# Kernel optimization log

Hardware: AMD Instinct MI355X
Metric: run time of the kernel (lower is better)

Reference implementation:

```python
import jax, jax.numpy as jnp
import numpy as np

N = 100000   # num nodes
E = 1600000  # num edges
D = 256      # input feature dim (dataset.num_features)


def setup_inputs() -> dict:
    key = jax.random.key(0)
    ks = jax.random.split(key, 10)

    def w(k, fan_in, fan_out):
        return jax.random.normal(k, (fan_in, fan_out), jnp.float32) / jnp.sqrt(fan_in)

    return {
        "x": jax.random.normal(ks[0], (N, D), jnp.float32),
        "edge_index": jax.random.randint(ks[1], (2, E), 0, N, jnp.int32),
        "W1": w(ks[2], D, 128),   "b1": jnp.zeros((128,), jnp.float32),
        "W2": w(ks[3], 128, 128), "b2": jnp.zeros((128,), jnp.float32),
        "W3": w(ks[4], 128, 64),  "b3": jnp.zeros((64,), jnp.float32),
        "W4": w(ks[5], 64, 32),   "b4": jnp.zeros((32,), jnp.float32),
    }


def _gcn_norm(edge_index, n):
    # GCNConv default: add self-loops, symmetric deg^-1/2 normalization
    loops = jnp.arange(n, dtype=edge_index.dtype)
    src = jnp.concatenate([edge_index[0], loops])
    dst = jnp.concatenate([edge_index[1], loops])
    deg = jax.ops.segment_sum(jnp.ones_like(dst, jnp.float32), dst, num_segments=n)
    dinv = jnp.where(deg > 0, jax.lax.rsqrt(deg), 0.0)
    norm = dinv[src] * dinv[dst]  # [E+N]
    return src, dst, norm


def _gcn_layer(x, W, b, src, dst, norm, n):
    h = x @ W                          # [N, out]
    msg = h[src] * norm[:, None]       # gather + scale: [E+N, out]
    agg = jax.ops.segment_sum(msg, dst, num_segments=n)  # scatter-add
    return agg + b


def reference(x, edge_index, W1, b1, W2, b2, W3, b3, W4, b4):
    n = x.shape[0]
    src, dst, norm = _gcn_norm(edge_index, n)
    h = jax.nn.relu(_gcn_layer(x, W1, b1, src, dst, norm, n))
    h = jax.nn.relu(_gcn_layer(h, W2, b2, src, dst, norm, n))
    h = jax.nn.relu(_gcn_layer(h, W3, b3, src, dst, norm, n))
    return _gcn_layer(h, W4, b4, src, dst, norm, n)  # encode() output z: [N, 32]
```

## Files before the change

### kernel.cpp

```cpp
#include <hip/hip_runtime.h>

#define CDIV(a,b) (((a)+(b)-1)/(b))
#define BUK_SHIFT 10
#define EPB 4096

typedef float f32x4 __attribute__((ext_vector_type(4)));
typedef short short8 __attribute__((ext_vector_type(8)));
typedef _Float16 h16x8 __attribute__((ext_vector_type(8)));


__device__ inline unsigned short rne_bf16(float f) {
    unsigned int u = __builtin_bit_cast(unsigned int, f);
    u += 0x7FFFu + ((u >> 16) & 1u);
    return (unsigned short)(u >> 16);
}

struct BF16Pair { short hi, lo; };

__device__ inline BF16Pair split_bf16(float f) {
    unsigned short h = rne_bf16(f);
    float fh = __builtin_bit_cast(float, (unsigned int)h << 16);
    BF16Pair p;
    p.hi = (short)h;
    p.lo = (short)rne_bf16(f - fh);
    return p;
}


__global__ __launch_bounds__(256) void bkt_hist_kernel(const int* __restrict__ dst,
                                                       int* __restrict__ hcnt,
                                                       int E, int nbuk, int nblk) {
    __shared__ int lh[128];
    int t = threadIdx.x;
    for (int i = t; i < nbuk; i += 256) lh[i] = 0;
    __syncthreads();
    int base = blockIdx.x * EPB;
    int end = min(base + EPB, E);
    for (int e = base + t; e < end; e += 256)
        atomicAdd(&lh[dst[e] >> BUK_SHIFT], 1);
    __syncthreads();
    for (int i = t; i < nbuk; i += 256) hcnt[i * nblk + blockIdx.x] = lh[i];
}

__global__ __launch_bounds__(1024) void scan_flat_kernel(int* a, int n) {
    __shared__ int s[1024];
    int t = threadIdx.x;
    int per = (n + 1023) / 1024;
    int start = t * per, end = min(start + per, n);
    int sum = 0;
    for (int i = start; i < end; ++i) sum += a[i];
    s[t] = sum;
    __syncthreads();
    for (int off = 1; off < 1024; off <<= 1) {
        int x = (t >= off) ? s[t - off] : 0;
        __syncthreads();
        s[t] += x;
        __syncthreads();
    }
    int run = s[t] - sum;
    for (int i = start; i < end; ++i) { int v = a[i]; a[i] = run; run += v; }
}

__global__ __launch_bounds__(256) void bkt_scatter_kernel(const int* __restrict__ src,
                                                          const int* __restrict__ dst,
                                                          const int* __restrict__ obk,
                                                          unsigned long long* __restrict__ ebuf,
                                                          int E, int nbuk, int nblk) {
    __shared__ int cur[128];
    int t = threadIdx.x;
    for (int i = t; i < nbuk; i += 256) cur[i] = obk[i * nblk + blockIdx.x];
    __syncthreads();
    int base = blockIdx.x * EPB;
    int end = min(base + EPB, E);
    for (int e = base + t; e < end; e += 256) {
        int d = dst[e], s = src[e];
        int b = d >> BUK_SHIFT;
        int pos = atomicAdd(&cur[b], 1);
        ebuf[pos] = ((unsigned long long)(unsigned)d << 32) | (unsigned)s;
    }
}

__global__ __launch_bounds__(1024) void bucket_csr_kernel(const unsigned long long* __restrict__ ebuf,
                                                          const int* __restrict__ hcnt,
                                                          int* __restrict__ rp,
                                                          float* __restrict__ dinv,
                                                          int* __restrict__ col,
                                                          int E, int N, int nbuk, int nblk) {
    __shared__ int lh[1024];
    __shared__ int lsc[1024];
    const int b = blockIdx.x;
    const int t = threadIdx.x;
    lh[t] = 0;
    __syncthreads();
    const int st = hcnt[b * nblk];
    const int en = (b + 1 < nbuk) ? hcnt[(b + 1) * nblk] : E;
    for (int e = st + t; e < en; e += 1024)
        atomicAdd(&lh[((int)(unsigned)(ebuf[e] >> 32)) & 1023], 1);
    __syncthreads();
    const int deg = lh[t];
    lsc[t] = deg;
    __syncthreads();
    for (int off = 1; off < 1024; off <<= 1) {
        int x = (t >= off) ? lsc[t - off] : 0;
        __syncthreads();
        lsc[t] += x;
        __syncthreads();
    }
    const int excl = lsc[t] - deg;
    const int node = (b << BUK_SHIFT) + t;
    if (node < N) {
        rp[node] = st + excl;
        dinv[node] = rsqrtf((float)deg + 1.0f);
    }
    if (b == 0 && t == 0) rp[N] = E;
    __syncthreads();
    lh[t] = st + excl;
    __syncthreads();
    for (int e = st + t; e < en; e += 1024) {
        unsigned long long r = ebuf[e];
        int d = (int)(unsigned)(r >> 32);
        int pos = atomicAdd(&lh[d & 1023], 1);
        col[pos] = (int)(unsigned)(r & 0xFFFFFFFFull);
    }
}


template<int K, int F>
__global__ void wprep_kernel(const float* __restrict__ W, short* __restrict__ whi,
                             short* __restrict__ wlo) {
    constexpr int CB = F / 16;
    int idx = blockIdx.x * 256 + threadIdx.x;
    if (idx >= K * F) return;
    int e = idx & 7;
    int lane = (idx >> 3) & 63;
    int fc = idx >> 9;
    int kb = fc / CB, cb = fc % CB;
    int k = kb * 32 + (lane >> 4) * 8 + e;
    int colv = cb * 16 + (lane & 15);
    BF16Pair p = split_bf16(W[k * F + colv]);
    whi[idx] = p.hi;
    wlo[idx] = p.lo;
}


template<int K, int F, typename AT>
__global__ __launch_bounds__(256) void mfma_gemm(const AT* __restrict__ A,
                                                 const short* __restrict__ Whi,
                                                 const short* __restrict__ Wlo,
                                                 const float* __restrict__ dinv,
                                                 _Float16* __restrict__ H, int N) {
    constexpr int CB = F / 16;
    constexpr int KB = K / 32;
    constexpr int HCH = CB * 64;
    constexpr int CHUNKS = HCH * 2;
    constexpr int CPT = (CHUNKS + 255) / 256;

    __shared__ __align__(16) short Bs[2][CB * 1024];

    const int tid = threadIdx.x;
    const int wid = tid >> 6, lane = tid & 63;
    const int rowf = lane & 15;
    const int kgrp = lane >> 4;
    const long long row0 = (long long)blockIdx.x * 64 + wid * 16;

    f32x4 acc[CB] = {};
    short8 breg[CPT];
    float fvaC[8], fvaN[8];

    auto stage_issue = [&](int kb) {
#pragma unroll
        for (int i = 0; i < CPT; ++i) {
            int c = tid + i * 256;
            if (CHUNKS < 256 && c >= CHUNKS) continue;
            const short* p = (c < HCH) ? (Whi + (size_t)kb * (CB * 512) + (size_t)c * 8)
                                       : (Wlo + (size_t)kb * (CB * 512) + (size_t)(c - HCH) * 8);
            breg[i] = *(const short8*)p;
        }
    };
    auto stage_write = [&](int b) {
#pragma unroll
        for (int i = 0; i < CPT; ++i) {
            int c = tid + i * 256;
            if (CHUNKS < 256 && c >= CHUNKS) continue;
            *(short8*)&Bs[b][(size_t)c * 8] = breg[i];
        }
    };
    auto a_load = [&](float (&dst)[8], int kb) {
        long long r = row0 + rowf;
        if (r < N) {
            const AT* ap = A + (size_t)r * K + kb * 32 + kgrp * 8;
            if constexpr (sizeof(AT) == 4) {
                float4 f0 = ((const float4*)ap)[0];
                float4 f1 = ((const float4*)ap)[1];
                dst[0]=f0.x; dst[1]=f0.y; dst[2]=f0.z; dst[3]=f0.w;
                dst[4]=f1.x; dst[5]=f1.y; dst[6]=f1.z; dst[7]=f1.w;
            } else {
                h16x8 hv = *(const h16x8*)ap;
#pragma unroll
                for (int j = 0; j < 8; ++j) dst[j] = (float)hv[j];
            }
        } else {
#pragma unroll
            for (int j = 0; j < 8; ++j) dst[j] = 0.f;
        }
    };

    stage_issue(0);
    a_load(fvaC, 0);

    for (int kb = 0; kb < KB; ++kb) {
        const int b = kb & 1;
        stage_write(b);
        if (kb + 1 < KB) stage_issue(kb + 1);
        asm volatile("s_waitcnt lgkmcnt(0)" ::: "memory");
        __builtin_amdgcn_s_barrier();
        __builtin_amdgcn_sched_barrier(0);
        if (kb + 1 < KB) a_load(fvaN, kb + 1);

        short8 ahi, alo;
#pragma unroll
        for (int j = 0; j < 8; ++j) {
            BF16Pair p = split_bf16(fvaC[j]);
            ahi[j] = p.hi;
            alo[j] = p.lo;
        }
#pragma unroll
        for (int cb = 0; cb < CB; ++cb) {
            short8 bhi = *(const short8*)&Bs[b][((size_t)cb * 64 + lane) * 8];
            short8 blo = *(const short8*)&Bs[b][CB * 512 + ((size_t)cb * 64 + lane) * 8];
            acc[cb] = __builtin_amdgcn_mfma_f32_16x16x32_bf16(ahi, bhi, acc[cb], 0, 0, 0);
            acc[cb] = __builtin_amdgcn_mfma_f32_16x16x32_bf16(alo, bhi, acc[cb], 0, 0, 0);
            acc[cb] = __builtin_amdgcn_mfma_f32_16x16x32_bf16(ahi, blo, acc[cb], 0, 0, 0);
        }
#pragma unroll
        for (int j = 0; j < 8; ++j) fvaC[j] = fvaN[j];
    }

    const int rsub = (lane >> 4) * 4;
    long long rbase = row0 + rsub;
    float dv[4];
#pragma unroll
    for (int j = 0; j < 4; ++j) dv[j] = (rbase + j < N) ? dinv[rbase + j] : 0.f;
#pragma unroll
    for (int cb = 0; cb < CB; ++cb) {
        int colv = cb * 16 + rowf;
#pragma unroll
        for (int j = 0; j < 4; ++j) {
            long long r = rbase + j;
            if (r < N) H[(size_t)r * F + colv] = (_Float16)(acc[cb][j] * dv[j]);
        }
    }
}


template<int F, bool RELU, typename OutT>
__global__ __launch_bounds__(256) void agg_kernel(const _Float16* __restrict__ hs,
                                                  const int* __restrict__ rp,
                                                  const int* __restrict__ col,
                                                  const float* __restrict__ dinv,
                                                  const float* __restrict__ bias,
                                                  OutT* __restrict__ out, int N) {
    constexpr int LPN = F / 8;
    constexpr int NPB = 256 / LPN;
    const int tid = threadIdx.x;
    const int lane = tid % LPN;
    const int node = blockIdx.x * NPB + tid / LPN;
    if (node >= N) return;

    const int f0 = lane * 8;
    const _Float16* hbase = hs + f0;

    float acc[8];
    {
        h16x8 sv = *(const h16x8*)(hbase + (size_t)node * F);
#pragma unroll
        for (int v = 0; v < 8; ++v) acc[v] = (float)sv[v];
    }

    int e = rp[node];
    const int e1 = rp[node + 1];
    for (; e + 4 <= e1; e += 4) {
        int s0 = col[e], s1 = col[e + 1], s2 = col[e + 2], s3 = col[e + 3];
        h16x8 v0 = *(const h16x8*)(hbase + (size_t)s0 * F);
        h16x8 v1 = *(const h16x8*)(hbase + (size_t)s1 * F);
        h16x8 v2 = *(const h16x8*)(hbase + (size_t)s2 * F);
        h16x8 v3 = *(const h16x8*)(hbase + (size_t)s3 * F);
#pragma unroll
        for (int v = 0; v < 8; ++v)
            acc[v] += ((float)v0[v] + (float)v1[v]) + ((float)v2[v] + (float)v3[v]);
    }
    for (; e < e1; ++e) {
        h16x8 v0 = *(const h16x8*)(hbase + (size_t)col[e] * F);
#pragma unroll
        for (int v = 0; v < 8; ++v) acc[v] += (float)v0[v];
    }

    const float self = dinv[node];
    OutT* op = out + (size_t)node * F + f0;
    const float* bp = bias + f0;
#pragma unroll
    for (int v = 0; v < 8; ++v) {
        float r = fmaf(acc[v], self, bp[v]);
        if (RELU) r = fmaxf(r, 0.f);
        op[v] = (OutT)r;
    }
}


extern "C" void kernel_launch(void* const* d_in, const int* in_sizes, int n_in,
                              void* d_out, int out_size, void* d_ws, size_t ws_size,
                              hipStream_t stream) {
    const float* x  = (const float*)d_in[0];
    const int*   ei = (const int*)d_in[1];
    const float* W1 = (const float*)d_in[2];
    const float* b1 = (const float*)d_in[3];
    const float* W2 = (const float*)d_in[4];
    const float* b2 = (const float*)d_in[5];
    const float* W3 = (const float*)d_in[6];
    const float* b3 = (const float*)d_in[7];
    const float* W4 = (const float*)d_in[8];
    const float* b4 = (const float*)d_in[9];

    const int N = in_sizes[0] / 256;
    const int E = in_sizes[1] / 2;
    const int* src = ei;
    const int* dst = ei + E;

    const int nbuk = ((N - 1) >> BUK_SHIFT) + 1;
    const int nblk = CDIV(E, EPB);

    char* base = (char*)d_ws;
    size_t o = 0;
    auto alloc = [&](size_t bytes) { char* p = base + o; o += (bytes + 255) & ~(size_t)255; return p; };
    int*   rp   = (int*)  alloc(sizeof(int) * (N + 1));
    float* dinv = (float*)alloc(sizeof(float) * N);
    int*   col  = (int*)  alloc(sizeof(int) * E);
    int*   hcnt = (int*)  alloc(sizeof(int) * (size_t)nbuk * nblk);
    unsigned long long* ebuf = (unsigned long long*)alloc(sizeof(unsigned long long) * E);
    short* w1h  = (short*)alloc(sizeof(short) * 256 * 128);
    short* w1l  = (short*)alloc(sizeof(short) * 256 * 128);
    short* w2h  = (short*)alloc(sizeof(short) * 128 * 128);
    short* w2l  = (short*)alloc(sizeof(short) * 128 * 128);
    short* w3h  = (short*)alloc(sizeof(short) * 128 * 64);
    short* w3l  = (short*)alloc(sizeof(short) * 128 * 64);
    short* w4h  = (short*)alloc(sizeof(short) * 64 * 32);
    short* w4l  = (short*)alloc(sizeof(short) * 64 * 32);
    _Float16* hsbuf = (_Float16*)alloc(sizeof(_Float16) * (size_t)N * 128);
    _Float16* zsbuf = (_Float16*)alloc(sizeof(_Float16) * (size_t)N * 128);
    float* out  = (float*)d_out;

    wprep_kernel<256, 128><<<CDIV(256 * 128, 256), 256, 0, stream>>>(W1, w1h, w1l);
    wprep_kernel<128, 128><<<CDIV(128 * 128, 256), 256, 0, stream>>>(W2, w2h, w2l);
    wprep_kernel<128, 64><<<CDIV(128 * 64, 256), 256, 0, stream>>>(W3, w3h, w3l);
    wprep_kernel<64, 32><<<CDIV(64 * 32, 256), 256, 0, stream>>>(W4, w4h, w4l);

    bkt_hist_kernel<<<nblk, 256, 0, stream>>>(dst, hcnt, E, nbuk, nblk);
    scan_flat_kernel<<<1, 1024, 0, stream>>>(hcnt, nbuk * nblk);
    bkt_scatter_kernel<<<nblk, 256, 0, stream>>>(src, dst, hcnt, ebuf, E, nbuk, nblk);

    bucket_csr_kernel<<<nbuk, 1024, 0, stream>>>(ebuf, hcnt, rp, dinv, col, E, N, nbuk, nblk);

    const int GG = CDIV(N, 64);

    mfma_gemm<256, 128, float><<<GG, 256, 0, stream>>>(x, w1h, w1l, dinv, hsbuf, N);
    agg_kernel<128, true, _Float16><<<CDIV(N, 16), 256, 0, stream>>>(hsbuf, rp, col, dinv, b1, zsbuf, N);

    mfma_gemm<128, 128, _Float16><<<GG, 256, 0, stream>>>(zsbuf, w2h, w2l, dinv, hsbuf, N);
    agg_kernel<128, true, _Float16><<<CDIV(N, 16), 256, 0, stream>>>(hsbuf, rp, col, dinv, b2, zsbuf, N);

    mfma_gemm<128, 64, _Float16><<<GG, 256, 0, stream>>>(zsbuf, w3h, w3l, dinv, hsbuf, N);
    agg_kernel<64, true, _Float16><<<CDIV(N, 32), 256, 0, stream>>>(hsbuf, rp, col, dinv, b3, zsbuf, N);

    mfma_gemm<64, 32, _Float16><<<GG, 256, 0, stream>>>(zsbuf, w4h, w4l, dinv, hsbuf, N);
    agg_kernel<32, false, float><<<CDIV(N, 64), 256, 0, stream>>>(hsbuf, rp, col, dinv, b4, out, N);
}
```

Measured before the change: 367.2 us.

## Fuse neighbor aggregation with next layer GEMM in a single kernel

Adds a fused kernel that gathers and sums neighbor features for a 64-node tile, applies normalization, bias and ReLU, and stores the result in a swizzled shared-memory tile. The tile is then fed straight into split-bf16 MFMA against the next layer's weights. This replaces three agg+gemm kernel pairs, removing the intermediate write and re-read of the aggregated activations and three launches. The trade-off is that each block does the irregular gather with fewer nodes per block, and the gather and GEMM phases are serialized within it, which may hurt latency hiding.

Measured after the change: 371.4 us. About the same (+1.1%).

```diff
diff --git a/kernel.cpp b/kernel.cpp
--- a/kernel.cpp
+++ b/kernel.cpp
@@ -79,6 +79,7 @@
         ebuf[pos] = ((unsigned long long)(unsigned)d << 32) | (unsigned)s;
     }
 }
+
 
 __global__ __launch_bounds__(1024) void bucket_csr_kernel(const unsigned long long* __restrict__ ebuf,
                                                           const int* __restrict__ hcnt,
@@ -238,6 +239,131 @@
 
     const int rsub = (lane >> 4) * 4;
     long long rbase = row0 + rsub;
+    float dv[4];
+#pragma unroll
+    for (int j = 0; j < 4; ++j) dv[j] = (rbase + j < N) ? dinv[rbase + j] : 0.f;
+#pragma unroll
+    for (int cb = 0; cb < CB; ++cb) {
+        int colv = cb * 16 + rowf;
+#pragma unroll
+        for (int j = 0; j < 4; ++j) {
+            long long r = rbase + j;
+            if (r < N) H[(size_t)r * F + colv] = (_Float16)(acc[cb][j] * dv[j]);
+        }
+    }
+}
+
+
+template<int KIN, int F>
+__global__ __launch_bounds__(256) void fused_agg_gemm(const _Float16* __restrict__ hs,
+                                                      const int* __restrict__ rp,
+                                                      const int* __restrict__ col,
+                                                      const float* __restrict__ dinv,
+                                                      const float* __restrict__ biasIn,
+                                                      const short* __restrict__ Whi,
+                                                      const short* __restrict__ Wlo,
+                                                      _Float16* __restrict__ H, int N) {
+    constexpr int CHK = KIN / 8;
+    constexpr int LPN = KIN / 8;
+    constexpr int NPB = 256 / LPN;
+    constexpr int ITERS = 64 / NPB;
+    constexpr int CB = F / 16;
+    constexpr int KB = KIN / 32;
+    constexpr int HCH = CB * 64;
+
+    __shared__ __align__(16) _Float16 Zt[64 * KIN];
+    __shared__ __align__(16) short Bs[CB * 1024];
+
+    const int tid = threadIdx.x;
+    const int base = blockIdx.x * 64;
+
+    for (int it = 0; it < ITERS; ++it) {
+        const int rl = it * NPB + tid / LPN;
+        const int node = base + rl;
+        const int lane16 = tid % LPN;
+        const int f0 = lane16 * 8;
+        const int sch = lane16 ^ (rl & (CHK - 1));
+        _Float16* zp = &Zt[rl * KIN + sch * 8];
+        if (node < N) {
+            const _Float16* hbase = hs + f0;
+            float acc[8];
+            {
+                h16x8 sv = *(const h16x8*)(hbase + (size_t)node * KIN);
+#pragma unroll
+                for (int v = 0; v < 8; ++v) acc[v] = (float)sv[v];
+            }
+            int e = rp[node];
+            const int e1 = rp[node + 1];
+            for (; e + 4 <= e1; e += 4) {
+                int s0 = col[e], s1 = col[e + 1], s2 = col[e + 2], s3 = col[e + 3];
+                h16x8 v0 = *(const h16x8*)(hbase + (size_t)s0 * KIN);
+                h16x8 v1 = *(const h16x8*)(hbase + (size_t)s1 * KIN);
+                h16x8 v2 = *(const h16x8*)(hbase + (size_t)s2 * KIN);
+                h16x8 v3 = *(const h16x8*)(hbase + (size_t)s3 * KIN);
+#pragma unroll
+                for (int v = 0; v < 8; ++v)
+                    acc[v] += ((float)v0[v] + (float)v1[v]) + ((float)v2[v] + (float)v3[v]);
+            }
+            for (; e < e1; ++e) {
+                h16x8 v0 = *(const h16x8*)(hbase + (size_t)col[e] * KIN);
+#pragma unroll
+                for (int v = 0; v < 8; ++v) acc[v] += (float)v0[v];
+            }
+            const float self = dinv[node];
+            h16x8 r;
+#pragma unroll
+            for (int v = 0; v < 8; ++v) {
+                float t = fmaf(acc[v], self, biasIn[f0 + v]);
+                r[v] = (_Float16)fmaxf(t, 0.f);
+            }
+            *(h16x8*)zp = r;
+        } else {
+            short8 z8 = {0,0,0,0,0,0,0,0};
+            *(short8*)zp = z8;
+        }
+    }
+    __syncthreads();
+
+    const int wid = tid >> 6, lane = tid & 63;
+    const int rowf = lane & 15;
+    const int kgrp = lane >> 4;
+    const int rl = wid * 16 + rowf;
+
+    f32x4 acc[CB] = {};
+
+    for (int kb = 0; kb < KB; ++kb) {
+        if (kb) __syncthreads();
+        constexpr int CPT = (HCH * 2) / 256;
+#pragma unroll
+        for (int i = 0; i < CPT; ++i) {
+            int c = tid + i * 256;
+            const short* p = (c < HCH) ? (Whi + (size_t)kb * (CB * 512) + (size_t)c * 8)
+                                       : (Wlo + (size_t)kb * (CB * 512) + (size_t)(c - HCH) * 8);
+            *(short8*)&Bs[(size_t)c * 8] = *(const short8*)p;
+        }
+        __syncthreads();
+
+        const int sch = (kb * 4 + kgrp) ^ (rl & (CHK - 1));
+        h16x8 av = *(const h16x8*)&Zt[rl * KIN + sch * 8];
+        short8 ahi, alo;
+#pragma unroll
+        for (int j = 0; j < 8; ++j) {
+            BF16Pair p = split_bf16((float)av[j]);
+            ahi[j] = p.hi;
+            alo[j] = p.lo;
+        }
+#pragma unroll
+        for (int cb = 0; cb < CB; ++cb) {
+            short8 bhi = *(const short8*)&Bs[((size_t)cb * 64 + lane) * 8];
+            short8 blo = *(const short8*)&Bs[CB * 512 + ((size_t)cb * 64 + lane) * 8];
+            acc[cb] = __builtin_amdgcn_mfma_f32_16x16x32_bf16(ahi, bhi, acc[cb], 0, 0, 0);
+            acc[cb] = __builtin_amdgcn_mfma_f32_16x16x32_bf16(alo, bhi, acc[cb], 0, 0, 0);
+            acc[cb] = __builtin_amdgcn_mfma_f32_16x16x32_bf16(ahi, blo, acc[cb], 0, 0, 0);
+        }
+    }
+
+    const int rsub = (lane >> 4) * 4;
+    long long rbase = (long long)base + wid * 16 + rsub;
     float dv[4];
 #pragma unroll
     for (int j = 0; j < 4; ++j) dv[j] = (rbase + j < N) ? dinv[rbase + j] : 0.f;
@@ -345,8 +471,8 @@
     short* w3l  = (short*)alloc(sizeof(short) * 128 * 64);
     short* w4h  = (short*)alloc(sizeof(short) * 64 * 32);
     short* w4l  = (short*)alloc(sizeof(short) * 64 * 32);
-    _Float16* hsbuf = (_Float16*)alloc(sizeof(_Float16) * (size_t)N * 128);
-    _Float16* zsbuf = (_Float16*)alloc(sizeof(_Float16) * (size_t)N * 128);
+    _Float16* hsA = (_Float16*)alloc(sizeof(_Float16) * (size_t)N * 128);
+    _Float16* hsB = (_Float16*)alloc(sizeof(_Float16) * (size_t)N * 128);
     float* out  = (float*)d_out;
 
     wprep_kernel<256, 128><<<CDIV(256 * 128, 256), 256, 0, stream>>>(W1, w1h, w1l);
@@ -357,20 +483,17 @@
     bkt_hist_kernel<<<nblk, 256, 0, stream>>>(dst, hcnt, E, nbuk, nblk);
     scan_flat_kernel<<<1, 1024, 0, stream>>>(hcnt, nbuk * nblk);
     bkt_scatter_kernel<<<nblk, 256, 0, stream>>>(src, dst, hcnt, ebuf, E, nbuk, nblk);
-
     bucket_csr_kernel<<<nbuk, 1024, 0, stream>>>(ebuf, hcnt, rp, dinv, col, E, N, nbuk, nblk);
 
     const int GG = CDIV(N, 64);
 
-    mfma_gemm<256, 128, float><<<GG, 256, 0, stream>>>(x, w1h, w1l, dinv, hsbuf, N);
-    agg_kernel<128, true, _Float16><<<CDIV(N, 16), 256, 0, stream>>>(hsbuf, rp, col, dinv, b1, zsbuf, N);
-
-    mfma_gemm<128, 128, _Float16><<<GG, 256, 0, stream>>>(zsbuf, w2h, w2l, dinv, hsbuf, N);
-    agg_kernel<128, true, _Float16><<<CDIV(N, 16), 256, 0, stream>>>(hsbuf, rp, col, dinv, b2, zsbuf, N);
-
-    mfma_gemm<128, 64, _Float16><<<GG, 256, 0, stream>>>(zsbuf, w3h, w3l, dinv, hsbuf, N);
-    agg_kernel<64, true, _Float16><<<CDIV(N, 32), 256, 0, stream>>>(hsbuf, rp, col, dinv, b3, zsbuf, N);
-
-    mfma_gemm<64, 32, _Float16><<<GG, 256, 0, stream>>>(zsbuf, w4h, w4l, dinv, hsbuf, N);
-    agg_kernel<32, false, float><<<CDIV(N, 64), 256, 0, stream>>>(hsbuf, rp, col, dinv, b4, out, N);
-}
+    mfma_gemm<256, 128, float><<<GG, 256, 0, stream>>>(x, w1h, w1l, dinv, hsA, N);
+
+    fused_agg_gemm<128, 128><<<GG, 256, 0, stream>>>(hsA, rp, col, dinv, b1, w2h, w2l, hsB, N);
+
+    fused_agg_gemm<128, 64><<<GG, 256, 0, stream>>>(hsB, rp, col, dinv, b2, w3h, w3l, hsA, N);
+
+    fused_agg_gemm<64, 32><<<GG, 256, 0, stream>>>(hsA, rp, col, dinv, b3, w4h, w4l, hsB, N);
+
+    agg_kernel<32, false, float><<<CDIV(N, 64), 256, 0, stream>>>(hsB, rp, col, dinv, b4, out, N);
+}
```

## Split aggregation into per-feature-slice blocks to shrink gather working set

Applied to the files above, without the earlier changes.

Replaces the aggregation kernel so that each block handles 128 nodes but only one 16-feature slice, with two threads per node and adjacent blocks covering different slices of the same nodes. The goal is a smaller gathered working set per wave of blocks and better cache locality across slices. In exchange each edge index is reread once per slice, there are more blocks, and each gather fetches only 32 bytes, which costs more memory transactions per feature.

Measured after the change: 810.8 us. +120.8%, slower.

```diff
diff --git a/kernel.cpp b/kernel.cpp
--- a/kernel.cpp
+++ b/kernel.cpp
@@ -79,6 +79,7 @@
         ebuf[pos] = ((unsigned long long)(unsigned)d << 32) | (unsigned)s;
     }
 }
+
 
 __global__ __launch_bounds__(1024) void bucket_csr_kernel(const unsigned long long* __restrict__ ebuf,
                                                           const int* __restrict__ hcnt,
@@ -254,20 +255,18 @@
 
 
 template<int F, bool RELU, typename OutT>
-__global__ __launch_bounds__(256) void agg_kernel(const _Float16* __restrict__ hs,
-                                                  const int* __restrict__ rp,
-                                                  const int* __restrict__ col,
-                                                  const float* __restrict__ dinv,
-                                                  const float* __restrict__ bias,
-                                                  OutT* __restrict__ out, int N) {
-    constexpr int LPN = F / 8;
-    constexpr int NPB = 256 / LPN;
-    const int tid = threadIdx.x;
-    const int lane = tid % LPN;
-    const int node = blockIdx.x * NPB + tid / LPN;
+__global__ __launch_bounds__(256) void agg_slice_kernel(const _Float16* __restrict__ hs,
+                                                        const int* __restrict__ rp,
+                                                        const int* __restrict__ col,
+                                                        const float* __restrict__ dinv,
+                                                        const float* __restrict__ bias,
+                                                        OutT* __restrict__ out, int N) {
+    constexpr int SLICES = F / 16;
+    const int slice = blockIdx.x & (SLICES - 1);
+    const int node = (int)(blockIdx.x / SLICES) * 128 + (threadIdx.x >> 1);
     if (node >= N) return;
 
-    const int f0 = lane * 8;
+    const int f0 = slice * 16 + (threadIdx.x & 1) * 8;
     const _Float16* hbase = hs + f0;
 
     float acc[8];
@@ -345,8 +344,8 @@
     short* w3l  = (short*)alloc(sizeof(short) * 128 * 64);
     short* w4h  = (short*)alloc(sizeof(short) * 64 * 32);
     short* w4l  = (short*)alloc(sizeof(short) * 64 * 32);
-    _Float16* hsbuf = (_Float16*)alloc(sizeof(_Float16) * (size_t)N * 128);
-    _Float16* zsbuf = (_Float16*)alloc(sizeof(_Float16) * (size_t)N * 128);
+    _Float16* hsA = (_Float16*)alloc(sizeof(_Float16) * (size_t)N * 128);
+    _Float16* hsB = (_Float16*)alloc(sizeof(_Float16) * (size_t)N * 128);
     float* out  = (float*)d_out;
 
     wprep_kernel<256, 128><<<CDIV(256 * 128, 256), 256, 0, stream>>>(W1, w1h, w1l);
@@ -357,20 +356,20 @@
     bkt_hist_kernel<<<nblk, 256, 0, stream>>>(dst, hcnt, E, nbuk, nblk);
     scan_flat_kernel<<<1, 1024, 0, stream>>>(hcnt, nbuk * nblk);
     bkt_scatter_kernel<<<nblk, 256, 0, stream>>>(src, dst, hcnt, ebuf, E, nbuk, nblk);
-
     bucket_csr_kernel<<<nbuk, 1024, 0, stream>>>(ebuf, hcnt, rp, dinv, col, E, N, nbuk, nblk);
 
     const int GG = CDIV(N, 64);
-
-    mfma_gemm<256, 128, float><<<GG, 256, 0, stream>>>(x, w1h, w1l, dinv, hsbuf, N);
-    agg_kernel<128, true, _Float16><<<CDIV(N, 16), 256, 0, stream>>>(hsbuf, rp, col, dinv, b1, zsbuf, N);
-
-    mfma_gemm<128, 128, _Float16><<<GG, 256, 0, stream>>>(zsbuf, w2h, w2l, dinv, hsbuf, N);
-    agg_kernel<128, true, _Float16><<<CDIV(N, 16), 256, 0, stream>>>(hsbuf, rp, col, dinv, b2, zsbuf, N);
-
-    mfma_gemm<128, 64, _Float16><<<GG, 256, 0, stream>>>(zsbuf, w3h, w3l, dinv, hsbuf, N);
-    agg_kernel<64, true, _Float16><<<CDIV(N, 32), 256, 0, stream>>>(hsbuf, rp, col, dinv, b3, zsbuf, N);
-
-    mfma_gemm<64, 32, _Float16><<<GG, 256, 0, stream>>>(zsbuf, w4h, w4l, dinv, hsbuf, N);
-    agg_kernel<32, false, float><<<CDIV(N, 64), 256, 0, stream>>>(hsbuf, rp, col, dinv, b4, out, N);
-}
+    const int AG = CDIV(N, 128);
+
+    mfma_gemm<256, 128, float><<<GG, 256, 0, stream>>>(x, w1h, w1l, dinv, hsA, N);
+    agg_slice_kernel<128, true, _Float16><<<AG * 8, 256, 0, stream>>>(hsA, rp, col, dinv, b1, hsB, N);
+
+    mfma_gemm<128, 128, _Float16><<<GG, 256, 0, stream>>>(hsB, w2h, w2l, dinv, hsA, N);
+    agg_slice_kernel<128, true, _Float16><<<AG * 8, 256, 0, stream>>>(hsA, rp, col, dinv, b2, hsB, N);
+
+    mfma_gemm<128, 64, _Float16><<<GG, 256, 0, stream>>>(hsB, w3h, w3l, dinv, hsA, N);
+    agg_slice_kernel<64, true, _Float16><<<AG * 4, 256, 0, stream>>>(hsA, rp, col, dinv, b3, hsB, N);
+
+    mfma_gemm<64, 32, _Float16><<<GG, 256, 0, stream>>>(hsB, w4h, w4l, dinv, hsA, N);
+    agg_slice_kernel<32, false, float><<<AG * 2, 256, 0, stream>>>(hsA, rp, col, dinv, b4, out, N);
+}
```
